# Kernel tuning notes

Measured on AMD Instinct MI355X. Metric: run time of the kernel, lower is better.

## Reference

```python
import jax, jax.numpy as jnp
import numpy as np

NDIM = 3
RADIUS = 0.2
N_POINT = 1024
N_SAMPLE = 32
D_INPUT = 64
D_HIDDEN = [64, 128, 256]
B, N = 8, 16384


def setup_inputs() -> dict:
    key = jax.random.key(0)
    ks = jax.random.split(key, 8)
    xyz = jax.random.uniform(ks[0], (B, NDIM, N), dtype=jnp.float32)
    points = jax.random.normal(ks[1], (B, D_INPUT, N), dtype=jnp.float32)
    # pointwise conv (kernel 1x1) weights: [out, in] plus bias [out]
    c_in = D_INPUT + NDIM
    inp = {"xyz": xyz, "points": points}
    for i, c_out in enumerate(D_HIDDEN):
        scale = 1.0 / np.sqrt(c_in)
        inp[f"w{i}"] = jax.random.uniform(ks[2 + 2 * i], (c_out, c_in), dtype=jnp.float32, minval=-scale, maxval=scale)
        inp[f"b{i}"] = jax.random.uniform(ks[3 + 2 * i], (c_out,), dtype=jnp.float32, minval=-scale, maxval=scale)
        c_in = c_out
    return inp


def farthest_point_sample(xyz):
    # xyz: [B, N, 3] -> idx [B, n_point]; deterministic, first index seeds (fps_method='first')
    b, n, _ = xyz.shape

    def step(carry, _):
        dist, farthest = carry  # [B, N], [B]
        centroid = jnp.take_along_axis(xyz, farthest[:, None, None], axis=1)  # [B,1,3]
        d = jnp.sum((xyz - centroid) ** 2, axis=-1)  # [B,N]
        dist = jnp.minimum(dist, d)
        return (dist, jnp.argmax(dist, axis=-1)), farthest

    init = (jnp.full((b, n), jnp.inf, xyz.dtype), jnp.zeros((b,), jnp.int32))
    _, idx = jax.lax.scan(step, init, None, length=N_POINT)
    return idx.T.astype(jnp.int32)  # [B, n_point]


def ball_query(new_xyz, xyz):
    # new_xyz: [B,S,3], xyz: [B,N,3] -> idx [B,S,K]
    n = xyz.shape[1]
    sqr = jnp.sum((new_xyz[:, :, None, :] - xyz[:, None, :, :]) ** 2, axis=-1)  # [B,S,N]
    cand = jnp.where(sqr > RADIUS * RADIUS, n, jnp.arange(n, dtype=jnp.int32))
    idx = jnp.sort(cand, axis=-1)[:, :, :N_SAMPLE]
    first = idx[:, :, :1]
    return jnp.where(idx == n, first, idx)


def sample_and_group(xyz, points):
    # xyz: [B,N,3], points: [B,N,D]
    fps_idx = farthest_point_sample(xyz)                      # [B,S]
    new_xyz = jax.vmap(lambda a, i: a[i])(xyz, fps_idx)       # [B,S,3]
    idx = jax.lax.stop_gradient(ball_query(jax.lax.stop_gradient(new_xyz), jax.lax.stop_gradient(xyz)))  # [B,S,K]
    grouped_xyz = jax.vmap(lambda a, i: a[i])(xyz, idx)       # [B,S,K,3]
    grouped_xyz_norm = grouped_xyz - new_xyz[:, :, None, :]
    grouped_points = jax.vmap(lambda a, i: a[i])(points, idx) # [B,S,K,D]
    new_points = jnp.concatenate([grouped_xyz_norm, grouped_points], axis=-1)  # [B,S,K,3+D]
    return new_xyz, new_points


def reference(xyz, points, w0, b0, w1, b1, w2, b2):
    # xyz: [B,3,N], points: [B,D,N]
    xyz_t = jnp.transpose(xyz, (0, 2, 1))      # [B,N,3]
    pts_t = jnp.transpose(points, (0, 2, 1))   # [B,N,D]
    _, new_points = sample_and_group(xyz_t, pts_t)      # [B,S,K,C]
    x = jnp.transpose(new_points, (0, 3, 2, 1))          # [B,C,K,S]
    for w, b in ((w0, b0), (w1, b1), (w2, b2)):
        x = jax.nn.silu(jnp.einsum('oc,bcks->boks', w, x) + b[None, :, None, None])
    return jnp.mean(x, axis=2)                            # [B, d_hidden[-1], S]
```

## Files before the change

kernel.cpp:

```cpp
#include <hip/hip_runtime.h>
#include <math.h>

#define NPTS 16384
#define NCTR 1024
#define BATCH 8
#define NCELL 512

typedef unsigned long long u64;
typedef unsigned int u32;

__device__ __forceinline__ float sq_dist(float x, float y, float z,
                                         float cx, float cy, float cz) {
  float dx = __fsub_rn(x, cx);
  float dy = __fsub_rn(y, cy);
  float dz = __fsub_rn(z, cz);
  return __fadd_rn(__fadd_rn(__fmul_rn(dx, dx), __fmul_rn(dy, dy)), __fmul_rn(dz, dz));
}

__device__ __forceinline__ float silu_f(float x) {
  return x / (1.0f + __expf(-x));
}

__device__ __forceinline__ u64 kmax(u64 a, u64 b) { return a > b ? a : b; }

__device__ __forceinline__ int morton_cell(float x, float y, float z) {
  int mx = min(7, max(0, (int)(x * 8.0f)));
  int my = min(7, max(0, (int)(y * 8.0f)));
  int mz = min(7, max(0, (int)(z * 8.0f)));
  int m = 0;
#pragma unroll
  for (int k = 0; k < 3; ++k) {
    m |= ((mx >> k) & 1) << (3 * k + 2);
    m |= ((my >> k) & 1) << (3 * k + 1);
    m |= ((mz >> k) & 1) << (3 * k + 0);
  }
  return m;
}

__global__ __launch_bounds__(1024) void sort_kernel(
    const float* __restrict__ xyz, float* __restrict__ sxg,
    float* __restrict__ syg, float* __restrict__ szg, int* __restrict__ sog) {
  const int b = blockIdx.x, t = threadIdx.x;
  const float* X = xyz + (size_t)b * 3 * NPTS;
  const float* Y = X + NPTS;
  const float* Z = X + 2 * NPTS;
  __shared__ int cnt[NCELL];
  __shared__ int off[NCELL];
  __shared__ int start[NCELL];
  __shared__ int so_l[NPTS];
  for (int e = t; e < NCELL; e += 1024) cnt[e] = 0;
  __syncthreads();
#pragma unroll
  for (int j = 0; j < 16; ++j) {
    const int n = t + (j << 10);
    atomicAdd(&cnt[morton_cell(X[n], Y[n], Z[n])], 1);
  }
  __syncthreads();
  if (t < NCELL) off[t] = cnt[t];
  __syncthreads();
  for (int d = 1; d < NCELL; d <<= 1) {
    int v = 0;
    if (t < NCELL) { v = off[t]; if (t >= d) v += off[t - d]; }
    __syncthreads();
    if (t < NCELL) off[t] = v;
    __syncthreads();
  }
  if (t < NCELL) { off[t] -= cnt[t]; start[t] = off[t]; }
  __syncthreads();
  for (int j = 0; j < 16; ++j) {
    const int n = t + (j << 10);
    const int pos = atomicAdd(&off[morton_cell(X[n], Y[n], Z[n])], 1);
    so_l[pos] = n;
    __syncthreads();
  }
  if (t < NCELL) {
    const int s0 = start[t], k = cnt[t];
    for (int i2 = 1; i2 < k; ++i2) {
      const int key = so_l[s0 + i2];
      int j2 = i2 - 1;
      while (j2 >= 0 && so_l[s0 + j2] > key) {
        so_l[s0 + j2 + 1] = so_l[s0 + j2];
        --j2;
      }
      so_l[s0 + j2 + 1] = key;
    }
  }
  __syncthreads();
  float* sx = sxg + (size_t)b * NPTS;
  float* sy = syg + (size_t)b * NPTS;
  float* sz = szg + (size_t)b * NPTS;
  int* so = sog + (size_t)b * NPTS;
#pragma unroll
  for (int j = 0; j < 16; ++j) {
    const int pos = t + (j << 10);
    const int n = so_l[pos];
    so[pos] = n;
    sx[pos] = X[n];
    sy[pos] = Y[n];
    sz[pos] = Z[n];
  }
}

#define CH_LIST(F) \
  F(0,a0)  F(1,a1)  F(2,a2)  F(3,a3)  F(4,a0)  F(5,a1)  F(6,a2)  F(7,a3)  \
  F(8,a0)  F(9,a1)  F(10,a2) F(11,a3) F(12,a0) F(13,a1) F(14,a2) F(15,a3)

__global__ __launch_bounds__(1024)
void fps_kernel(const float* __restrict__ xyz, const float* __restrict__ sxg,
                const float* __restrict__ syg, const float* __restrict__ szg,
                const int* __restrict__ sog, int* __restrict__ fps_idx) {
  const int b = blockIdx.x;
  const int t = threadIdx.x;
  const int w = t >> 6, lane = t & 63;
  const float* X = xyz + (size_t)b * 3 * NPTS;
  const float* Y = X + NPTS;
  const float* Z = X + 2 * NPTS;
  const float* SX = sxg + (size_t)b * NPTS;
  const float* SY = syg + (size_t)b * NPTS;
  const float* SZ = szg + (size_t)b * NPTS;
  const int* SO = sog + (size_t)b * NPTS;

  __shared__ float sxy[2 * NPTS];
  __shared__ __align__(16) u64 slot[3][2];
  __shared__ float s_zw[3][16];
  __shared__ int fps_lds[NCTR];

#define DECL_CH(c, acc) float z##c, d##c; u32 lo##c;
  CH_LIST(DECL_CH)
#undef DECL_CH

  const int wbase = (w << 6) + lane;

  float bmnx = __builtin_inff(), bmxx = -__builtin_inff();
  float bmny = __builtin_inff(), bmxy = -__builtin_inff();
  float bmnz = __builtin_inff(), bmxz = -__builtin_inff();

#define INIT_CH(c, acc)                                         \
  {                                                             \
    const int p = ((c) << 10) + wbase;                          \
    const float xv = SX[p], yv = SY[p], zv = SZ[p];             \
    sxy[2 * p] = xv; sxy[2 * p + 1] = yv;                       \
    z##c = zv;                                                  \
    const int o = SO[p];                                        \
    lo##c = ((u32)(16383 - o) << 14) | (u32)p;                  \
    d##c = __builtin_inff();                                    \
    float mnx = xv, mxx = xv, mny = yv, mxy = yv;               \
    float mnz = zv, mxz = zv;                                   \
    _Pragma("unroll")                                           \
    for (int off = 32; off >= 1; off >>= 1) {                   \
      mnx = fminf(mnx, __shfl_xor(mnx, off));                   \
      mxx = fmaxf(mxx, __shfl_xor(mxx, off));                   \
      mny = fminf(mny, __shfl_xor(mny, off));                   \
      mxy = fmaxf(mxy, __shfl_xor(mxy, off));                   \
      mnz = fminf(mnz, __shfl_xor(mnz, off));                   \
      mxz = fmaxf(mxz, __shfl_xor(mxz, off));                   \
    }                                                           \
    if (lane == c) {                                            \
      bmnx = mnx; bmxx = mxx; bmny = mny;                       \
      bmxy = mxy; bmnz = mnz; bmxz = mxz;                       \
    }                                                           \
  }
  CH_LIST(INIT_CH)
#undef INIT_CH

#define PIN_CH(c, acc) asm volatile("" : "+v"(z##c));
  CH_LIST(PIN_CH)
#undef PIN_CH

  if (t < 6) slot[t / 2][t & 1] = 0ull;
  if (t == 0) fps_lds[0] = 0;
  __syncthreads();

  float cx = X[0], cy = Y[0], cz = Z[0];
  float gd = __builtin_inff();
  u64 gkey = 0ull;
  float gz = 0.0f;
  int wmaxch = 0;

#define MK(c) ((((u64)__float_as_uint(d##c)) << 32) | (u64)lo##c)
#define KSEL(ka, za, kb, zb, ko, zo)          \
  {                                           \
    const u64 ka_ = (ka), kb_ = (kb);         \
    const bool g_ = ka_ > kb_;                \
    ko = g_ ? ka_ : kb_;                      \
    zo = g_ ? (za) : (zb);                    \
  }

  for (int i = 1; i < NCTR; ++i) {
    const float ux = fmaxf(fmaxf(__fsub_rn(bmnx, cx), __fsub_rn(cx, bmxx)), 0.0f);
    const float uy = fmaxf(fmaxf(__fsub_rn(bmny, cy), __fsub_rn(cy, bmxy)), 0.0f);
    const float uz = fmaxf(fmaxf(__fsub_rn(bmnz, cz), __fsub_rn(cz, bmxz)), 0.0f);
    const float lb = __fadd_rn(__fadd_rn(__fmul_rn(ux, ux), __fmul_rn(uy, uy)),
                               __fmul_rn(uz, uz));
    const u32 mask = (u32)__ballot(!(__fmul_rn(lb, 0.9999f) >= gd));
    if (mask != 0u) {
      if (__builtin_popcount(mask) >= 6) {
#define UPDU_CH(c, acc)                                                  \
        {                                                                \
          const float2 xy =                                              \
              *(const float2*)(sxy + 2 * (((c) << 10) + wbase));         \
          const float dd = sq_dist(xy.x, xy.y, z##c, cx, cy, cz);        \
          d##c = fminf(d##c, dd);                                        \
        }
        CH_LIST(UPDU_CH)
#undef UPDU_CH
      } else {
#define UPDG_CH(c, acc)                                                  \
        if (mask & (1u << (c))) {                                        \
          const float2 xy =                                              \
              *(const float2*)(sxy + 2 * (((c) << 10) + wbase));         \
          float dd = sq_dist(xy.x, xy.y, z##c, cx, cy, cz);              \
          asm volatile("" : "+v"(dd));                                   \
          d##c = fminf(d##c, dd);                                        \
        }
        CH_LIST(UPDG_CH)
#undef UPDG_CH
      }
      if ((mask >> wmaxch) & 1u) {
        u64 m0, m1, m2, m3, m4, m5, m6, m7, q0, q1, q2, q3, h0, h1, kk;
        float n0, n1, n2, n3, n4, n5, n6, n7, r0, r1, r2, r3, e0, e1, bz;
        KSEL(MK(0), z0, MK(1), z1, m0, n0)    KSEL(MK(2), z2, MK(3), z3, m1, n1)
        KSEL(MK(4), z4, MK(5), z5, m2, n2)    KSEL(MK(6), z6, MK(7), z7, m3, n3)
        KSEL(MK(8), z8, MK(9), z9, m4, n4)    KSEL(MK(10), z10, MK(11), z11, m5, n5)
        KSEL(MK(12), z12, MK(13), z13, m6, n6) KSEL(MK(14), z14, MK(15), z15, m7, n7)
        KSEL(m0, n0, m1, n1, q0, r0)  KSEL(m2, n2, m3, n3, q1, r1)
        KSEL(m4, n4, m5, n5, q2, r2)  KSEL(m6, n6, m7, n7, q3, r3)
        KSEL(q0, r0, q1, r1, h0, e0)  KSEL(q2, r2, q3, r3, h1, e1)
        KSEL(h0, e0, h1, e1, kk, bz)
#pragma unroll
        for (int off = 32; off >= 1; off >>= 1) {
          const u64 ok = __shfl_xor(kk, off);
          const float oz = __shfl_xor(bz, off);
          const bool g_ = ok > kk;
          kk = g_ ? ok : kk;
          bz = g_ ? oz : bz;
        }
        gkey = kk;
        gz = bz;
        gd = __uint_as_float((u32)(gkey >> 32));
        wmaxch = (int)(((u32)gkey >> 10) & 15u);
      }
    }
    const int si = i % 3;
    if (lane == 0) {
      s_zw[si][w] = gz;
      atomicMax(&slot[si][w & 1], gkey);
    }
    if (t == 0) {
      const int nsi = si == 2 ? 0 : si + 1;
      slot[nsi][0] = 0ull;
      slot[nsi][1] = 0ull;
    }
    __syncthreads();

    const u64 m = kmax(slot[si][0], slot[si][1]);
    const u32 lowb = (u32)m;
    const int pw = (int)(lowb & 0x3FFFu);
    if (t == 0) fps_lds[i] = 16383 - (int)((lowb >> 14) & 0x3FFFu);

    const int pu = __builtin_amdgcn_readfirstlane(pw);
    const float2 cxy = *(const float2*)(sxy + 2 * pu);
    cx = cxy.x;
    cy = cxy.y;
    cz = s_zw[si][(pu >> 6) & 15];
  }
#undef MK
#undef KSEL

  __syncthreads();
  for (int e = t; e < NCTR; e += 1024) fps_idx[b * NCTR + e] = fps_lds[e];
}

__global__ __launch_bounds__(256) void ballq_kernel(const float* __restrict__ xyz,
                                                    const int* __restrict__ fps_idx,
                                                    int* __restrict__ ball_idx) {
  const int gw = (blockIdx.x * 256 + threadIdx.x) >> 6;
  const int lane = threadIdx.x & 63;
  const int b = gw >> 10;
  const float* X = xyz + (size_t)b * 3 * NPTS;
  const float* Y = X + NPTS;
  const float* Z = X + 2 * NPTS;
  const int c = fps_idx[gw];
  const float cx = X[c], cy = Y[c], cz = Z[c];
  int* out = ball_idx + (size_t)gw * 32;
  const float R2 = 0.04f;

  int cnt = 0, first = -1;
  for (int base = 0; base < NPTS; base += 64) {
    const int j = base + lane;
    const float d = sq_dist(X[j], Y[j], Z[j], cx, cy, cz);
    const bool inb = !(d > R2);
    const unsigned long long m = __ballot(inb);
    if (first < 0 && m != 0ull) first = base + __ffsll(m) - 1;
    if (inb) {
      const int pos = cnt + __popcll(m & ((1ull << lane) - 1ull));
      if (pos < 32) out[pos] = j;
    }
    cnt += __popcll(m);
    if (cnt >= 32) break;
  }
  for (int k = cnt + lane; k < 32; k += 64) out[k] = first;
}

__global__ __launch_bounds__(256) void transpose_w_kernel(
    const float* __restrict__ w0, const float* __restrict__ w1,
    const float* __restrict__ w2, float* __restrict__ wt0,
    float* __restrict__ wt1, float* __restrict__ wt2) {
  const int t0 = blockIdx.x * 256 + threadIdx.x;
  const int stride = gridDim.x * 256;
  for (int e = t0; e < 64 * 67; e += stride) {
    int o = e / 67, c = e - o * 67;
    wt0[c * 64 + o] = w0[e];
  }
  for (int e = t0; e < 128 * 64; e += stride) {
    int o = e >> 6, c = e & 63;
    wt1[c * 128 + o] = w1[e];
  }
  for (int e = t0; e < 256 * 128; e += stride) {
    int o = e >> 7, c = e & 127;
    wt2[c * 256 + o] = w2[e];
  }
}

__global__ __launch_bounds__(256, 4) void mlp_kernel(
    const float* __restrict__ xyz, const float* __restrict__ points,
    const int* __restrict__ fps_idx, const int* __restrict__ ball_idx,
    const float* __restrict__ wt0, const float* __restrict__ b0,
    const float* __restrict__ wt1, const float* __restrict__ b1,
    const float* __restrict__ wt2, const float* __restrict__ b2,
    float* __restrict__ out) {
  const int bx = blockIdx.x, b = blockIdx.y, t = threadIdx.x;
  const int s = (bx & 7) * 128 + (bx >> 3);

  __shared__ float A0[67 * 36];
  __shared__ float A1[64 * 36];
  __shared__ float A2[128 * 36];
  __shared__ int jidx[32];
  __shared__ float ctr[3];

  const int g = b * NCTR + s;

  if (t < 32) jidx[t] = ball_idx[(size_t)g * 32 + t];
  if (t < 3) ctr[t] = xyz[((size_t)b * 3 + t) * NPTS + fps_idx[g]];
  __syncthreads();

  for (int e = t; e < 67 * 32; e += 256) {
    int c = e >> 5, k = e & 31;
    int j = jidx[k];
    float v;
    if (c < 3)
      v = xyz[((size_t)b * 3 + c) * NPTS + j] - ctr[c];
    else
      v = points[((size_t)b * 64 + (c - 3)) * NPTS + j];
    A0[c * 36 + k] = v;
  }
  __syncthreads();

  {
    const int o0 = (t & 31) * 2;
    const int k0 = (t >> 5) * 4;
    const float2 bb = *(const float2*)(b0 + o0);
    float acc[4][2] = {{0.f, 0.f}, {0.f, 0.f}, {0.f, 0.f}, {0.f, 0.f}};
    for (int c = 0; c < 67; ++c) {
      const float4 a = *(const float4*)(A0 + c * 36 + k0);
      const float2 wv = *(const float2*)(wt0 + c * 64 + o0);
      acc[0][0] = fmaf(a.x, wv.x, acc[0][0]);
      acc[1][0] = fmaf(a.y, wv.x, acc[1][0]);
      acc[2][0] = fmaf(a.z, wv.x, acc[2][0]);
      acc[3][0] = fmaf(a.w, wv.x, acc[3][0]);
      acc[0][1] = fmaf(a.x, wv.y, acc[0][1]);
      acc[1][1] = fmaf(a.y, wv.y, acc[1][1]);
      acc[2][1] = fmaf(a.z, wv.y, acc[2][1]);
      acc[3][1] = fmaf(a.w, wv.y, acc[3][1]);
    }
    const float bbv[2] = {bb.x, bb.y};
#pragma unroll
    for (int i = 0; i < 2; ++i) {
      float4 r;
      r.x = silu_f(acc[0][i] + bbv[i]);
      r.y = silu_f(acc[1][i] + bbv[i]);
      r.z = silu_f(acc[2][i] + bbv[i]);
      r.w = silu_f(acc[3][i] + bbv[i]);
      *(float4*)(A1 + (o0 + i) * 36 + k0) = r;
    }
  }
  __syncthreads();

  {
    const int o0 = (t & 31) * 4;
    const int k0 = (t >> 5) * 4;
    const float4 bb = *(const float4*)(b1 + o0);
    float acc[4][4];
#pragma unroll
    for (int kk = 0; kk < 4; ++kk)
#pragma unroll
      for (int oo = 0; oo < 4; ++oo) acc[kk][oo] = 0.f;
    for (int c = 0; c < 64; ++c) {
      const float4 a = *(const float4*)(A1 + c * 36 + k0);
      const float4 w = *(const float4*)(wt1 + c * 128 + o0);
      const float av[4] = {a.x, a.y, a.z, a.w};
      const float wv[4] = {w.x, w.y, w.z, w.w};
#pragma unroll
      for (int kk = 0; kk < 4; ++kk)
#pragma unroll
        for (int oo = 0; oo < 4; ++oo)
          acc[kk][oo] = fmaf(av[kk], wv[oo], acc[kk][oo]);
    }
    const float bbv[4] = {bb.x, bb.y, bb.z, bb.w};
#pragma unroll
    for (int oo = 0; oo < 4; ++oo) {
      float4 r;
      r.x = silu_f(acc[0][oo] + bbv[oo]);
      r.y = silu_f(acc[1][oo] + bbv[oo]);
      r.z = silu_f(acc[2][oo] + bbv[oo]);
      r.w = silu_f(acc[3][oo] + bbv[oo]);
      *(float4*)(A2 + (o0 + oo) * 36 + k0) = r;
    }
  }
  __syncthreads();

  float* P = A1;
  const int o0 = (t & 31) * 2;
  const int k0 = (t >> 5) * 4;
  const int kg = t >> 5;
  for (int chunk = 0; chunk < 4; ++chunk) {
    const float2 bb = *(const float2*)(b2 + chunk * 64 + o0);
    float acc[4][2] = {{0.f, 0.f}, {0.f, 0.f}, {0.f, 0.f}, {0.f, 0.f}};
    for (int c = 0; c < 128; ++c) {
      const float4 a = *(const float4*)(A2 + c * 36 + k0);
      const float2 wv =
          *(const float2*)(wt2 + c * 256 + chunk * 64 + o0);
      acc[0][0] = fmaf(a.x, wv.x, acc[0][0]);
      acc[1][0] = fmaf(a.y, wv.x, acc[1][0]);
      acc[2][0] = fmaf(a.z, wv.x, acc[2][0]);
      acc[3][0] = fmaf(a.w, wv.x, acc[3][0]);
      acc[0][1] = fmaf(a.x, wv.y, acc[0][1]);
      acc[1][1] = fmaf(a.y, wv.y, acc[1][1]);
      acc[2][1] = fmaf(a.z, wv.y, acc[2][1]);
      acc[3][1] = fmaf(a.w, wv.y, acc[3][1]);
    }
    const float bbv[2] = {bb.x, bb.y};
#pragma unroll
    for (int i = 0; i < 2; ++i) {
      float sum = silu_f(acc[0][i] + bbv[i]) + silu_f(acc[1][i] + bbv[i]) +
                  silu_f(acc[2][i] + bbv[i]) + silu_f(acc[3][i] + bbv[i]);
      P[(o0 + i) * 9 + kg] = sum;
    }
    __syncthreads();
    if (t < 64) {
      float tot = 0.f;
#pragma unroll
      for (int q = 0; q < 8; ++q) tot += P[t * 9 + q];
      out[((size_t)b * 256 + chunk * 64 + t) * NCTR + s] = tot * (1.0f / 32.0f);
    }
    __syncthreads();
  }
}

extern "C" void kernel_launch(void* const* d_in, const int* in_sizes, int n_in,
                              void* d_out, int out_size, void* d_ws, size_t ws_size,
                              hipStream_t stream) {
  const float* xyz = (const float*)d_in[0];
  const float* points = (const float*)d_in[1];
  const float* w0 = (const float*)d_in[2];
  const float* b0 = (const float*)d_in[3];
  const float* w1 = (const float*)d_in[4];
  const float* b1 = (const float*)d_in[5];
  const float* w2 = (const float*)d_in[6];
  const float* b2 = (const float*)d_in[7];
  float* out = (float*)d_out;

  int* fps = (int*)d_ws;
  int* bidx = (int*)d_ws + 8192;
  float* wt0 = (float*)d_ws + 270336;
  float* wt1 = wt0 + 67 * 64;
  float* wt2 = wt1 + 64 * 128;
  float* sxg = (float*)d_ws + 315584;
  float* syg = sxg + BATCH * NPTS;
  float* szg = syg + BATCH * NPTS;
  int* sog = (int*)(szg + BATCH * NPTS);

  transpose_w_kernel<<<64, 256, 0, stream>>>(w0, w1, w2, wt0, wt1, wt2);
  sort_kernel<<<BATCH, 1024, 0, stream>>>(xyz, sxg, syg, szg, sog);
  fps_kernel<<<BATCH, 1024, 0, stream>>>(xyz, sxg, syg, szg, sog, fps);
  ballq_kernel<<<2048, 256, 0, stream>>>(xyz, fps, bidx);
  mlp_kernel<<<dim3(NCTR, BATCH), 256, 0, stream>>>(xyz, points, fps, bidx,
                                                    wt0, b0, wt1, b1, wt2, b2, out);
}
```

Baseline: 2.000 ms.

## Stage MLP weight chunks through shared memory instead of global reads

The MLP kernel now copies each layer's transposed weights in chunks into a shared buffer with padded strides, and the inner loops read weights from LDS rather than global memory. Output channels are split into smaller chunks (32 or 64) per pass, and each thread computes fewer outputs. Occupancy is lowered from 4 to 3 blocks per SM. This trades extra barriers, cooperative load passes and more shared memory for removing per-FMA global or L1 weight loads.

```diff
diff --git a/kernel.cpp b/kernel.cpp
--- a/kernel.cpp
+++ b/kernel.cpp
@@ -322,7 +322,7 @@
   }
 }
 
-__global__ __launch_bounds__(256, 4) void mlp_kernel(
+__global__ __launch_bounds__(256, 3) void mlp_kernel(
     const float* __restrict__ xyz, const float* __restrict__ points,
     const int* __restrict__ fps_idx, const int* __restrict__ ball_idx,
     const float* __restrict__ wt0, const float* __restrict__ b0,
@@ -332,13 +332,15 @@
   const int bx = blockIdx.x, b = blockIdx.y, t = threadIdx.x;
   const int s = (bx & 7) * 128 + (bx >> 3);
 
-  __shared__ float A0[67 * 36];
+  __shared__ float S[4623];
   __shared__ float A1[64 * 36];
   __shared__ float A2[128 * 36];
   __shared__ int jidx[32];
   __shared__ float ctr[3];
 
   const int g = b * NCTR + s;
+  float* A0 = S;
+  float* Wt0c = S + 67 * 36;
 
   if (t < 32) jidx[t] = ball_idx[(size_t)g * 32 + t];
   if (t < 3) ctr[t] = xyz[((size_t)b * 3 + t) * NPTS + fps_idx[g]];
@@ -354,16 +356,51 @@
       v = points[((size_t)b * 64 + (c - 3)) * NPTS + j];
     A0[c * 36 + k] = v;
   }
-  __syncthreads();
-
-  {
-    const int o0 = (t & 31) * 2;
-    const int k0 = (t >> 5) * 4;
-    const float2 bb = *(const float2*)(b0 + o0);
-    float acc[4][2] = {{0.f, 0.f}, {0.f, 0.f}, {0.f, 0.f}, {0.f, 0.f}};
+
+  const int ot = t & 31;
+  const int kg = t >> 5;
+  const int k0 = kg * 4;
+
+  for (int ch = 0; ch < 2; ++ch) {
+    __syncthreads();
+    for (int e = t; e < 67 * 32; e += 256) {
+      int c = e >> 5, o = e & 31;
+      Wt0c[c * 33 + o] = wt0[c * 64 + ch * 32 + o];
+    }
+    __syncthreads();
+    const int o = ch * 32 + ot;
+    const float bb = b0[o];
+    float a0 = 0.f, a1 = 0.f, a2 = 0.f, a3 = 0.f;
     for (int c = 0; c < 67; ++c) {
       const float4 a = *(const float4*)(A0 + c * 36 + k0);
-      const float2 wv = *(const float2*)(wt0 + c * 64 + o0);
+      const float wv = Wt0c[c * 33 + ot];
+      a0 = fmaf(a.x, wv, a0);
+      a1 = fmaf(a.y, wv, a1);
+      a2 = fmaf(a.z, wv, a2);
+      a3 = fmaf(a.w, wv, a3);
+    }
+    float4 r;
+    r.x = silu_f(a0 + bb);
+    r.y = silu_f(a1 + bb);
+    r.z = silu_f(a2 + bb);
+    r.w = silu_f(a3 + bb);
+    *(float4*)(A1 + o * 36 + k0) = r;
+  }
+
+  float* Wt1c = S;
+  for (int ch = 0; ch < 2; ++ch) {
+    __syncthreads();
+    for (int e = t; e < 64 * 64; e += 256) {
+      int c = e >> 6, o = e & 63;
+      Wt1c[c * 68 + o] = wt1[c * 128 + ch * 64 + o];
+    }
+    __syncthreads();
+    const int o0 = ch * 64 + 2 * ot;
+    const float2 bb = *(const float2*)(b1 + o0);
+    float acc[4][2] = {{0.f, 0.f}, {0.f, 0.f}, {0.f, 0.f}, {0.f, 0.f}};
+    for (int c = 0; c < 64; ++c) {
+      const float4 a = *(const float4*)(A1 + c * 36 + k0);
+      const float2 wv = *(const float2*)(Wt1c + c * 68 + 2 * ot);
       acc[0][0] = fmaf(a.x, wv.x, acc[0][0]);
       acc[1][0] = fmaf(a.y, wv.x, acc[1][0]);
       acc[2][0] = fmaf(a.z, wv.x, acc[2][0]);
@@ -381,79 +418,40 @@
       r.y = silu_f(acc[1][i] + bbv[i]);
       r.z = silu_f(acc[2][i] + bbv[i]);
       r.w = silu_f(acc[3][i] + bbv[i]);
-      *(float4*)(A1 + (o0 + i) * 36 + k0) = r;
-    }
-  }
-  __syncthreads();
-
-  {
-    const int o0 = (t & 31) * 4;
-    const int k0 = (t >> 5) * 4;
-    const float4 bb = *(const float4*)(b1 + o0);
-    float acc[4][4];
-#pragma unroll
-    for (int kk = 0; kk < 4; ++kk)
-#pragma unroll
-      for (int oo = 0; oo < 4; ++oo) acc[kk][oo] = 0.f;
-    for (int c = 0; c < 64; ++c) {
-      const float4 a = *(const float4*)(A1 + c * 36 + k0);
-      const float4 w = *(const float4*)(wt1 + c * 128 + o0);
-      const float av[4] = {a.x, a.y, a.z, a.w};
-      const float wv[4] = {w.x, w.y, w.z, w.w};
-#pragma unroll
-      for (int kk = 0; kk < 4; ++kk)
-#pragma unroll
-        for (int oo = 0; oo < 4; ++oo)
-          acc[kk][oo] = fmaf(av[kk], wv[oo], acc[kk][oo]);
-    }
-    const float bbv[4] = {bb.x, bb.y, bb.z, bb.w};
-#pragma unroll
-    for (int oo = 0; oo < 4; ++oo) {
-      float4 r;
-      r.x = silu_f(acc[0][oo] + bbv[oo]);
-      r.y = silu_f(acc[1][oo] + bbv[oo]);
-      r.z = silu_f(acc[2][oo] + bbv[oo]);
-      r.w = silu_f(acc[3][oo] + bbv[oo]);
-      *(float4*)(A2 + (o0 + oo) * 36 + k0) = r;
-    }
-  }
-  __syncthreads();
-
+      *(float4*)(A2 + (o0 + i) * 36 + k0) = r;
+    }
+  }
+
+  float* Wt2c = S;
   float* P = A1;
-  const int o0 = (t & 31) * 2;
-  const int k0 = (t >> 5) * 4;
-  const int kg = t >> 5;
-  for (int chunk = 0; chunk < 4; ++chunk) {
-    const float2 bb = *(const float2*)(b2 + chunk * 64 + o0);
-    float acc[4][2] = {{0.f, 0.f}, {0.f, 0.f}, {0.f, 0.f}, {0.f, 0.f}};
+  for (int ch = 0; ch < 8; ++ch) {
+    __syncthreads();
+    for (int e = t; e < 128 * 32; e += 256) {
+      int c = e >> 5, o = e & 31;
+      Wt2c[c * 33 + o] = wt2[c * 256 + ch * 32 + o];
+    }
+    __syncthreads();
+    const int o = ch * 32 + ot;
+    const float bb = b2[o];
+    float a0 = 0.f, a1 = 0.f, a2 = 0.f, a3 = 0.f;
     for (int c = 0; c < 128; ++c) {
       const float4 a = *(const float4*)(A2 + c * 36 + k0);
-      const float2 wv =
-          *(const float2*)(wt2 + c * 256 + chunk * 64 + o0);
-      acc[0][0] = fmaf(a.x, wv.x, acc[0][0]);
-      acc[1][0] = fmaf(a.y, wv.x, acc[1][0]);
-      acc[2][0] = fmaf(a.z, wv.x, acc[2][0]);
-      acc[3][0] = fmaf(a.w, wv.x, acc[3][0]);
-      acc[0][1] = fmaf(a.x, wv.y, acc[0][1]);
-      acc[1][1] = fmaf(a.y, wv.y, acc[1][1]);
-      acc[2][1] = fmaf(a.z, wv.y, acc[2][1]);
-      acc[3][1] = fmaf(a.w, wv.y, acc[3][1]);
-    }
-    const float bbv[2] = {bb.x, bb.y};
-#pragma unroll
-    for (int i = 0; i < 2; ++i) {
-      float sum = silu_f(acc[0][i] + bbv[i]) + silu_f(acc[1][i] + bbv[i]) +
-                  silu_f(acc[2][i] + bbv[i]) + silu_f(acc[3][i] + bbv[i]);
-      P[(o0 + i) * 9 + kg] = sum;
-    }
-    __syncthreads();
-    if (t < 64) {
+      const float wv = Wt2c[c * 33 + ot];
+      a0 = fmaf(a.x, wv, a0);
+      a1 = fmaf(a.y, wv, a1);
+      a2 = fmaf(a.z, wv, a2);
+      a3 = fmaf(a.w, wv, a3);
+    }
+    const float sum = silu_f(a0 + bb) + silu_f(a1 + bb) +
+                      silu_f(a2 + bb) + silu_f(a3 + bb);
+    P[ot * 9 + kg] = sum;
+    __syncthreads();
+    if (t < 32) {
       float tot = 0.f;
 #pragma unroll
       for (int q = 0; q < 8; ++q) tot += P[t * 9 + q];
-      out[((size_t)b * 256 + chunk * 64 + t) * NCTR + s] = tot * (1.0f / 32.0f);
-    }
-    __syncthreads();
+      out[((size_t)b * 256 + ch * 32 + t) * NCTR + s] = tot * (1.0f / 32.0f);
+    }
   }
 }
 
```

Measured after the change: 1.999 ms. Within noise of the previous version (-0.1%).
